# Performance work log

Measured on AMD Instinct MI355X. Metric: run time of the kernel, lower is better.

The kernel has to match this reference:

```python
import jax, jax.numpy as jnp
import numpy as np

N = 500_000
H = 256
G = 4096
NUM_TIMESTEPS = 2


def setup_inputs() -> dict:
    key = jax.random.key(0)
    ks = jax.random.split(key, 12)
    s = 0.05
    x = jax.random.normal(ks[0], (N, H), dtype=jnp.float32)
    batch = jnp.sort(jax.random.randint(ks[1], (N,), 0, G, dtype=jnp.int64))
    return {
        "x": x,
        "gate_w1": jax.random.normal(ks[2], (H, H), dtype=jnp.float32) * s,
        "gate_b1": jax.random.normal(ks[3], (H,), dtype=jnp.float32) * s,
        "gate_w2": jax.random.normal(ks[4], (1, H), dtype=jnp.float32) * s,
        "gate_b2": jax.random.normal(ks[5], (1,), dtype=jnp.float32) * s,
        "gru_w_ih": jax.random.normal(ks[6], (3 * H, H), dtype=jnp.float32) * s,
        "gru_w_hh": jax.random.normal(ks[7], (3 * H, H), dtype=jnp.float32) * s,
        "gru_b_ih": jax.random.normal(ks[8], (3 * H,), dtype=jnp.float32) * s,
        "gru_b_hh": jax.random.normal(ks[9], (3 * H,), dtype=jnp.float32) * s,
        "batch": batch,
        "num_graphs": G,
    }


def _gru_cell(inp, h, w_ih, w_hh, b_ih, b_hh):
    # torch.nn.GRUCell semantics; gate order [r, z, n]
    gi = inp @ w_ih.T + b_ih
    gh = h @ w_hh.T + b_hh
    i_r, i_z, i_n = jnp.split(gi, 3, axis=-1)
    h_r, h_z, h_n = jnp.split(gh, 3, axis=-1)
    r = jax.nn.sigmoid(i_r + h_r)
    z = jax.nn.sigmoid(i_z + h_z)
    n = jnp.tanh(i_n + r * h_n)
    return (1.0 - z) * n + z * h


def reference(x, gate_w1, gate_b1, gate_w2, gate_b2,
              gru_w_ih, gru_w_hh, gru_b_ih, gru_b_hh,
              batch, num_graphs):
    counts = jax.ops.segment_sum(jnp.ones((x.shape[0],), x.dtype), batch,
                                 num_segments=num_graphs)
    denom = jnp.maximum(counts, 1.0)[:, None]  # empty graphs -> 0 mean

    def mean_pool(v):
        return jax.ops.segment_sum(v, batch, num_segments=num_graphs) / denom

    graph_repr = mean_pool(x)  # (G, H)
    for _ in range(NUM_TIMESTEPS):
        # gather per-node graph context (batch is sorted == node_to_graph)
        gate_input = x + graph_repr[batch]  # (N, H)
        hgate = jax.nn.relu(gate_input @ gate_w1.T + gate_b1)
        gate = jax.nn.sigmoid(hgate @ gate_w2.T + gate_b2)  # (N, 1)
        weighted_x = x * gate
        new_graph_repr = mean_pool(weighted_x)
        graph_repr = _gru_cell(new_graph_repr, graph_repr,
                               gru_w_ih, gru_w_hh, gru_b_ih, gru_b_hh)
        graph_repr = jax.nn.relu(graph_repr)
    return graph_repr
```

## Files before the change

kernel.cpp:

```cpp
#include <hip/hip_runtime.h>
#include <hip/hip_bf16.h>
#include <stdint.h>

#define H 256
#define G 4096
#define TK 32
#define TP0 128

typedef __attribute__((ext_vector_type(8))) short bf16x8;
typedef __attribute__((ext_vector_type(4))) float f32x4;

__device__ inline short f2bf(float f){
  union { float f; uint32_t u; } v; v.f = f;
  uint32_t r = (v.u + 0x7FFFu + ((v.u >> 16) & 1u)) >> 16;
  return (short)(uint16_t)r;
}
__device__ inline float bf2f(short s){
  union { float f; uint32_t u; } v; v.u = ((uint32_t)(uint16_t)s) << 16;
  return v.f;
}
__device__ inline uint32_t pk2(float lo, float hi){
  return (uint32_t)(uint16_t)f2bf(lo) | ((uint32_t)(uint16_t)f2bf(hi) << 16);
}
__device__ inline uint32_t pkfp8(float4 v){
  int u = __builtin_amdgcn_cvt_pk_fp8_f32(v.x, v.y, 0, false);
  u = __builtin_amdgcn_cvt_pk_fp8_f32(v.z, v.w, u, true);
  return (uint32_t)u;
}
__device__ inline float sigmoidf_(float x){ return 1.f / (1.f + __expf(-x)); }

__device__ inline void ldsbar(){
  asm volatile("s_waitcnt lgkmcnt(0)" ::: "memory");
  __builtin_amdgcn_s_barrier();
}

__global__ void conv_w(const float* __restrict__ w1, const float* __restrict__ wih,
                       const float* __restrict__ whh,
                       short* __restrict__ o1, short* __restrict__ oih, short* __restrict__ ohh,
                       uint8_t* __restrict__ w1q,
                       float* __restrict__ counts, float* __restrict__ pool){
  int i = blockIdx.x * 256 + threadIdx.x;
  if (i < H*H) o1[i] = f2bf(w1[i]);
  if (i < 3*H*H){ oih[i] = f2bf(wih[i]); ohh[i] = f2bf(whh[i]); }
  if (i < H*H/4){
    float4 v = *(const float4*)(w1 + (size_t)i*4);
    *(uint32_t*)(w1q + (size_t)i*4) = pkfp8(v);
  }
  if (i < G) counts[i] = 0.f;
  for (int j = i; j < G*H; j += 768*256) pool[j] = 0.f;
}

__global__ __launch_bounds__(512) __attribute__((amdgpu_waves_per_eu(2, 8)))
void k0_pool(const float* __restrict__ x, const int* __restrict__ batch,
             float* __restrict__ pool, float* __restrict__ counts,
             short* __restrict__ xbf, uint8_t* __restrict__ xq,
             float* __restrict__ sgate, int nNodes){
  __shared__ int   ng[TP0];
  __shared__ float Pacc[8][H];
  __shared__ float Cacc[8];
  __shared__ int   spanSh;

  const int t = threadIdx.x;
  const int base = blockIdx.x * TP0;
  const int c4 = (t & 63) * 4;
  const int r0 = (t >> 6) * 16;

  float4 v[16];
  #pragma unroll
  for (int i = 0; i < 16; ++i){
    int node = base + r0 + i;
    if (node < nNodes) v[i] = *(const float4*)(x + (size_t)node*H + c4);
    else v[i] = make_float4(0.f,0.f,0.f,0.f);
  }

  { int gi = blockIdx.x * 512 + t; if (gi < nNodes) sgate[gi] = 0.f; }

  if (t < TP0) ng[t] = (base + t < nNodes) ? batch[base + t] : -1;
  for (int u = t; u < 8*H; u += 512) ((float*)Pacc)[u] = 0.f;
  if (t < 8) Cacc[t] = 0.f;
  __syncthreads();

  if (t == 0){
    int lg = ng[0];
    if (base + TP0 <= nNodes) lg = ng[TP0-1];
    else { for (int i = TP0-1; i > 0; --i){ if (ng[i] >= 0){ lg = ng[i]; break; } } }
    spanSh = (ng[0] >= 0) ? (lg - ng[0]) : -1;
  }

  if (xbf){
    #pragma unroll
    for (int i = 0; i < 16; ++i){
      int node = base + r0 + i;
      if (node < nNodes){
        ushort4 o;
        o.x = (uint16_t)f2bf(v[i].x); o.y = (uint16_t)f2bf(v[i].y);
        o.z = (uint16_t)f2bf(v[i].z); o.w = (uint16_t)f2bf(v[i].w);
        *(ushort4*)(xbf + (size_t)node*H + c4) = o;
        *(uint32_t*)(xq + (size_t)node*H + c4) = pkfp8(v[i]);
      }
    }
  }
  __syncthreads();

  const int g0 = ng[0];
  const bool useLds = (spanSh >= 0) && (spanSh < 8);

  float ax=0.f, ay=0.f, az=0.f, aw=0.f;
  int cur = ng[r0];
  if (cur >= 0){
    #pragma unroll
    for (int i = 0; i < 16; ++i){
      int g = ng[r0 + i];
      if (g < 0) break;
      if (g != cur){
        if (useLds){
          atomicAdd(&Pacc[cur-g0][c4], ax);   atomicAdd(&Pacc[cur-g0][c4+1], ay);
          atomicAdd(&Pacc[cur-g0][c4+2], az); atomicAdd(&Pacc[cur-g0][c4+3], aw);
        } else {
          atomicAdd(&pool[(size_t)cur*H + c4], ax);   atomicAdd(&pool[(size_t)cur*H + c4+1], ay);
          atomicAdd(&pool[(size_t)cur*H + c4+2], az); atomicAdd(&pool[(size_t)cur*H + c4+3], aw);
        }
        ax=ay=az=aw=0.f; cur = g;
      }
      ax += v[i].x; ay += v[i].y; az += v[i].z; aw += v[i].w;
    }
    if (useLds){
      atomicAdd(&Pacc[cur-g0][c4], ax);   atomicAdd(&Pacc[cur-g0][c4+1], ay);
      atomicAdd(&Pacc[cur-g0][c4+2], az); atomicAdd(&Pacc[cur-g0][c4+3], aw);
    } else {
      atomicAdd(&pool[(size_t)cur*H + c4], ax);   atomicAdd(&pool[(size_t)cur*H + c4+1], ay);
      atomicAdd(&pool[(size_t)cur*H + c4+2], az); atomicAdd(&pool[(size_t)cur*H + c4+3], aw);
    }
  }
  if (t < TP0 && ng[t] >= 0){
    if (useLds) atomicAdd(&Cacc[ng[t]-g0], 1.f);
    else        atomicAdd(&counts[ng[t]], 1.f);
  }
  __syncthreads();

  if (useLds){
    int nr = spanSh + 1;
    for (int u = t; u < nr*H; u += 512){
      int r = u >> 8, c = u & 255;
      float vv = Pacc[r][c];
      if (vv != 0.f) atomicAdd(&pool[(size_t)(g0+r)*H + c], vv);
    }
    if (t < nr && Cacc[t] != 0.f) atomicAdd(&counts[g0 + t], Cacc[t]);
  }
}

__global__ __launch_bounds__(256) void kT2(float* __restrict__ pool,
    const float* __restrict__ counts, float* __restrict__ repr,
    const short* __restrict__ w1bf, const float* __restrict__ b1,
    uint32_t* __restrict__ hgp){
  __shared__ short Ar[16][H + 8];
  const int t    = threadIdx.x;
  const int wid  = t >> 6;
  const int lane = t & 63;
  const int l15  = lane & 15;
  const int l4   = lane >> 4;
  const int g0   = blockIdx.x * 16;

  for (int u = t; u < 16*32; u += 256){
    int row = u >> 5, cg = u & 31;
    int c0 = cg * 8;
    int g = g0 + row;
    float cnt = fmaxf(counts[g], 1.f);
    float4* pp = (float4*)(pool + (size_t)g*H + c0);
    float4 p0 = pp[0], p1 = pp[1];
    p0.x/=cnt; p0.y/=cnt; p0.z/=cnt; p0.w/=cnt;
    p1.x/=cnt; p1.y/=cnt; p1.z/=cnt; p1.w/=cnt;
    float4* rp = (float4*)(repr + (size_t)g*H + c0);
    rp[0] = p0; rp[1] = p1;
    pp[0] = make_float4(0.f,0.f,0.f,0.f);
    pp[1] = make_float4(0.f,0.f,0.f,0.f);
    bf16x8 o;
    o[0]=f2bf(p0.x); o[1]=f2bf(p0.y); o[2]=f2bf(p0.z); o[3]=f2bf(p0.w);
    o[4]=f2bf(p1.x); o[5]=f2bf(p1.y); o[6]=f2bf(p1.z); o[7]=f2bf(p1.w);
    *(bf16x8*)(&Ar[row][c0]) = o;
  }
  __syncthreads();

  f32x4 acc[4];
  #pragma unroll
  for (int i = 0; i < 4; ++i) acc[i] = (f32x4){0.f,0.f,0.f,0.f};
  #pragma unroll
  for (int kc = 0; kc < 8; ++kc){
    bf16x8 a = *(bf16x8*)(&Ar[l15][kc*32 + l4*8]);
    #pragma unroll
    for (int nt = 0; nt < 4; ++nt){
      int col = wid*64 + nt*16 + l15;
      bf16x8 b = *(const bf16x8*)(w1bf + (size_t)col*H + kc*32 + l4*8);
      acc[nt] = __builtin_amdgcn_mfma_f32_16x16x32_bf16(a, b, acc[nt], 0, 0, 0);
    }
  }
  const float b1v0 = b1[wid*64 + l15];
  const float b1v1 = b1[wid*64 + 16 + l15];
  const float b1v2 = b1[wid*64 + 32 + l15];
  const float b1v3 = b1[wid*64 + 48 + l15];
  #pragma unroll
  for (int j = 0; j < 4; ++j){
    int row = l4*4 + j;
    hgp[(size_t)(g0+row)*128 + wid*32 + l15]      = pk2(acc[0][j]+b1v0, acc[1][j]+b1v1);
    hgp[(size_t)(g0+row)*128 + wid*32 + 16 + l15] = pk2(acc[2][j]+b1v2, acc[3][j]+b1v3);
  }
}

__global__ __launch_bounds__(256) __attribute__((amdgpu_waves_per_eu(3, 4)))
void k1a_fp8(
    const uint8_t* __restrict__ xq, const int* __restrict__ batch,
    const uint32_t* __restrict__ hgp, const uint8_t* __restrict__ w1q,
    const float* __restrict__ w2, float* __restrict__ sgate,
    int nNodes, int nTiles, int nBlk){

  __shared__ uint8_t Ain[2][TK][H + 16];
  __shared__ int     ngS[2][TK];

  const int t    = threadIdx.x;
  const int wid  = t >> 6;
  const int lane = t & 63;
  const int l15  = lane & 15;
  const int l4   = lane >> 4;
  const int colB = wid*64;

  const int tile0 = (int)(((long long)blockIdx.x * nTiles) / nBlk);
  const int tile1 = (int)(((long long)(blockIdx.x+1) * nTiles) / nBlk);
  if (tile0 >= tile1) return;

  long BfA0[8], BfA1[8], BfB0[8], BfB1[8];
  {
    const uint8_t* wp = w1q + (size_t)(colB + l15)*H + l4*8;
    #pragma unroll
    for (int kc = 0; kc < 8; ++kc){
      BfA0[kc] = *(const long*)(wp + kc*32);
      BfA1[kc] = *(const long*)(wp + 16*H + kc*32);
      BfB0[kc] = *(const long*)(wp + 32*H + kc*32);
      BfB1[kc] = *(const long*)(wp + 48*H + kc*32);
    }
  }
  const float w2A0 = w2[colB + l15];
  const float w2A1 = w2[colB + 16 + l15];
  const float w2B0 = w2[colB + 32 + l15];
  const float w2B1 = w2[colB + 48 + l15];

  const int srow  = t >> 4;
  const int scolB = (t & 15) * 16;
  uint4 xv0, xv1;
  int ngv = -1;

  auto issueT = [&](int tile){
    int base = tile * TK;
    int n0 = base + srow, n1 = n0 + 16;
    xv0 = (n0 < nNodes) ? *(const uint4*)(xq + (size_t)n0*H + scolB) : make_uint4(0,0,0,0);
    xv1 = (n1 < nNodes) ? *(const uint4*)(xq + (size_t)n1*H + scolB) : make_uint4(0,0,0,0);
    if (t < TK){
      int node = base + t;
      ngv = (node < nNodes) ? batch[node] : -1;
    }
  };
  auto stageT = [&](int buf){
    *(uint4*)(&Ain[buf][srow][scolB])      = xv0;
    *(uint4*)(&Ain[buf][srow + 16][scolB]) = xv1;
    if (t < TK) ngS[buf][t] = ngv;
  };

  issueT(tile0);
  stageT(0);
  if (tile0 + 1 < tile1) issueT(tile0 + 1);

  int cur = 0;
  for (int tile = tile0; tile < tile1; ++tile, cur ^= 1){
    ldsbar();

    uint32_t hvp[2][4];
    #pragma unroll
    for (int r = 0; r < 2; ++r)
      #pragma unroll
      for (int j = 0; j < 4; ++j){
        int g = ngS[cur][r*16 + l4*4 + j];
        hvp[r][j] = (g >= 0) ? hgp[(size_t)g*128 + wid*32 + l15] : 0u;
      }

    f32x4 acc0[2], acc1[2];
    #pragma unroll
    for (int r = 0; r < 2; ++r){ acc0[r] = (f32x4){0.f,0.f,0.f,0.f}; acc1[r] = (f32x4){0.f,0.f,0.f,0.f}; }
    #pragma unroll
    for (int kc = 0; kc < 8; ++kc){
      #pragma unroll
      for (int r = 0; r < 2; ++r){
        long a = *(const long*)(&Ain[cur][r*16 + l15][kc*32 + l4*8]);
        acc0[r] = __builtin_amdgcn_mfma_f32_16x16x32_fp8_fp8(a, BfA0[kc], acc0[r], 0, 0, 0);
        acc1[r] = __builtin_amdgcn_mfma_f32_16x16x32_fp8_fp8(a, BfA1[kc], acc1[r], 0, 0, 0);
      }
    }

    if (tile + 1 < tile1){
      stageT(cur ^ 1);
      if (tile + 2 < tile1) issueT(tile + 2);
    }

    float p[2][4];
    #pragma unroll
    for (int r = 0; r < 2; ++r)
      #pragma unroll
      for (int j = 0; j < 4; ++j){
        float h0 = fmaxf(acc0[r][j] + bf2f((short)(uint16_t)(hvp[r][j] & 0xFFFFu)), 0.f);
        float h1 = fmaxf(acc1[r][j] + bf2f((short)(uint16_t)(hvp[r][j] >> 16)), 0.f);
        p[r][j] = w2A0*h0 + w2A1*h1;
      }

    #pragma unroll
    for (int r = 0; r < 2; ++r)
      #pragma unroll
      for (int j = 0; j < 4; ++j){
        int g = ngS[cur][r*16 + l4*4 + j];
        hvp[r][j] = (g >= 0) ? hgp[(size_t)g*128 + wid*32 + 16 + l15] : 0u;
      }
    #pragma unroll
    for (int r = 0; r < 2; ++r){ acc0[r] = (f32x4){0.f,0.f,0.f,0.f}; acc1[r] = (f32x4){0.f,0.f,0.f,0.f}; }
    #pragma unroll
    for (int kc = 0; kc < 8; ++kc){
      #pragma unroll
      for (int r = 0; r < 2; ++r){
        long a = *(const long*)(&Ain[cur][r*16 + l15][kc*32 + l4*8]);
        acc0[r] = __builtin_amdgcn_mfma_f32_16x16x32_fp8_fp8(a, BfB0[kc], acc0[r], 0, 0, 0);
        acc1[r] = __builtin_amdgcn_mfma_f32_16x16x32_fp8_fp8(a, BfB1[kc], acc1[r], 0, 0, 0);
      }
    }
    #pragma unroll
    for (int r = 0; r < 2; ++r)
      #pragma unroll
      for (int j = 0; j < 4; ++j){
        float h0 = fmaxf(acc0[r][j] + bf2f((short)(uint16_t)(hvp[r][j] & 0xFFFFu)), 0.f);
        float h1 = fmaxf(acc1[r][j] + bf2f((short)(uint16_t)(hvp[r][j] >> 16)), 0.f);
        p[r][j] += w2B0*h0 + w2B1*h1;
      }

    #pragma unroll
    for (int off = 1; off < 16; off <<= 1){
      #pragma unroll
      for (int r = 0; r < 2; ++r)
        #pragma unroll
        for (int j = 0; j < 4; ++j) p[r][j] += __shfl_xor(p[r][j], off);
    }
    if (l15 == 0){
      int base = tile * TK;
      #pragma unroll
      for (int r = 0; r < 2; ++r)
        #pragma unroll
        for (int j = 0; j < 4; ++j){
          int idx = r*16 + l4*4 + j;
          if (ngS[cur][idx] >= 0)
            atomicAdd(&sgate[base + idx], p[r][j]);
        }
    }
  }
}

template<bool BF>
__global__ __launch_bounds__(512) __attribute__((amdgpu_waves_per_eu(2, 8)))
void k1b_pool(
    const float* __restrict__ xf32, const short* __restrict__ xbf,
    const int* __restrict__ batch, float* __restrict__ sgate,
    const float* __restrict__ b2p, float* __restrict__ pool, int nNodes){

  __shared__ int   ng[TP0];
  __shared__ float gs[TP0];
  __shared__ float Pacc[8][H];
  __shared__ int   spanSh;

  const int t = threadIdx.x;
  const int base = blockIdx.x * TP0;
  const int c4 = (t & 63) * 4;
  const int r0 = (t >> 6) * 16;

  ushort4 u[16];
  float4  vf[16];
  #pragma unroll
  for (int i = 0; i < 16; ++i){
    int node = base + r0 + i;
    if constexpr (BF){
      u[i] = (node < nNodes) ? *(const ushort4*)(xbf + (size_t)node*H + c4)
                             : make_ushort4(0,0,0,0);
    } else {
      vf[i] = (node < nNodes) ? *(const float4*)(xf32 + (size_t)node*H + c4)
                              : make_float4(0.f,0.f,0.f,0.f);
    }
  }

  const float b2v = b2p[0];
  if (t < TP0){
    int node = base + t;
    if (node < nNodes){
      ng[t] = batch[node];
      gs[t] = sigmoidf_(sgate[node] + b2v);
      sgate[node] = 0.f;
    } else { ng[t] = -1; gs[t] = 0.f; }
  }
  for (int w = t; w < 8*H; w += 512) ((float*)Pacc)[w] = 0.f;
  __syncthreads();

  if (t == 0){
    int lg = ng[0];
    if (base + TP0 <= nNodes) lg = ng[TP0-1];
    else { for (int i = TP0-1; i > 0; --i){ if (ng[i] >= 0){ lg = ng[i]; break; } } }
    spanSh = (ng[0] >= 0) ? (lg - ng[0]) : -1;
  }
  __syncthreads();

  const int g0 = ng[0];
  const bool useLds = (spanSh >= 0) && (spanSh < 8);

  float ax=0.f, ay=0.f, az=0.f, aw=0.f;
  int cur = ng[r0];
  if (cur >= 0){
    #pragma unroll
    for (int i = 0; i < 16; ++i){
      int g = ng[r0 + i];
      if (g < 0) break;
      if (g != cur){
        if (useLds){
          atomicAdd(&Pacc[cur-g0][c4], ax);   atomicAdd(&Pacc[cur-g0][c4+1], ay);
          atomicAdd(&Pacc[cur-g0][c4+2], az); atomicAdd(&Pacc[cur-g0][c4+3], aw);
        } else {
          atomicAdd(&pool[(size_t)cur*H + c4], ax);   atomicAdd(&pool[(size_t)cur*H + c4+1], ay);
          atomicAdd(&pool[(size_t)cur*H + c4+2], az); atomicAdd(&pool[(size_t)cur*H + c4+3], aw);
        }
        ax=ay=az=aw=0.f; cur = g;
      }
      float gv = gs[r0 + i];
      if constexpr (BF){
        ax += gv * bf2f((short)u[i].x); ay += gv * bf2f((short)u[i].y);
        az += gv * bf2f((short)u[i].z); aw += gv * bf2f((short)u[i].w);
      } else {
        ax += gv * bf2f(f2bf(vf[i].x)); ay += gv * bf2f(f2bf(vf[i].y));
        az += gv * bf2f(f2bf(vf[i].z)); aw += gv * bf2f(f2bf(vf[i].w));
      }
    }
    if (useLds){
      atomicAdd(&Pacc[cur-g0][c4], ax);   atomicAdd(&Pacc[cur-g0][c4+1], ay);
      atomicAdd(&Pacc[cur-g0][c4+2], az); atomicAdd(&Pacc[cur-g0][c4+3], aw);
    } else {
      atomicAdd(&pool[(size_t)cur*H + c4], ax);   atomicAdd(&pool[(size_t)cur*H + c4+1], ay);
      atomicAdd(&pool[(size_t)cur*H + c4+2], az); atomicAdd(&pool[(size_t)cur*H + c4+3], aw);
    }
  }
  __syncthreads();

  if (useLds){
    int nr = spanSh + 1;
    for (int w = t; w < nr*H; w += 512){
      int r = w >> 8, c = w & 255;
      float vv = Pacc[r][c];
      if (vv != 0.f) atomicAdd(&pool[(size_t)(g0+r)*H + c], vv);
    }
  }
}

__global__ __launch_bounds__(256) __attribute__((amdgpu_waves_per_eu(3, 4)))
void k1a_gate_f32(
    const float* __restrict__ xf32, const int* __restrict__ batch,
    const uint32_t* __restrict__ hgp, const short* __restrict__ w1bf,
    const float* __restrict__ w2, float* __restrict__ sgate,
    int nNodes, int nTiles, int nChains){

  __shared__ short Ain[2][TK][H + 8];
  __shared__ int   ngS[2][TK];

  const int t    = threadIdx.x;
  const int wid  = t >> 6;
  const int lane = t & 63;
  const int l15  = lane & 15;
  const int l4   = lane >> 4;

  const int ch    = blockIdx.x >= nChains;
  const int chain = ch ? blockIdx.x - nChains : blockIdx.x;
  const int colB  = ch*128 + wid*32;
  const int hgcol = ch*64 + wid*16 + l15;

  const int tile0 = (int)(((long long)chain * nTiles) / nChains);
  const int tile1 = (int)(((long long)(chain+1) * nTiles) / nChains);
  if (tile0 >= tile1) return;

  bf16x8 Bf0[8], Bf1[8];
  {
    const short* wp0 = w1bf + (size_t)(colB + l15)*H + l4*8;
    #pragma unroll
    for (int kc = 0; kc < 8; ++kc){
      Bf0[kc] = *(const bf16x8*)(wp0 + kc*32);
      Bf1[kc] = *(const bf16x8*)(wp0 + 16*H + kc*32);
    }
  }
  const float w2v0 = w2[colB + l15];
  const float w2v1 = w2[colB + 16 + l15];

  const int srow = t >> 5;
  const int scol = (t & 31) * 8;
  float4 xf[4][2];
  int ngv = -1;

  auto issueT = [&](int tile){
    int base = tile * TK;
    #pragma unroll
    for (int q = 0; q < 4; ++q){
      int node = base + srow + q*8;
      if (node < nNodes){
        const float4* xp = (const float4*)(xf32 + (size_t)node*H + scol);
        xf[q][0] = xp[0]; xf[q][1] = xp[1];
      } else { xf[q][0] = make_float4(0.f,0.f,0.f,0.f); xf[q][1] = make_float4(0.f,0.f,0.f,0.f); }
    }
    if (t < TK){
      int node = base + t;
      ngv = (node < nNodes) ? batch[node] : -1;
    }
  };
  auto stageT = [&](int buf){
    #pragma unroll
    for (int q = 0; q < 4; ++q){
      bf16x8 o;
      float4 a = xf[q][0], c = xf[q][1];
      o[0]=f2bf(a.x); o[1]=f2bf(a.y); o[2]=f2bf(a.z); o[3]=f2bf(a.w);
      o[4]=f2bf(c.x); o[5]=f2bf(c.y); o[6]=f2bf(c.z); o[7]=f2bf(c.w);
      *(bf16x8*)(&Ain[buf][srow + q*8][scol]) = o;
    }
    if (t < TK) ngS[buf][t] = ngv;
  };

  issueT(tile0);
  stageT(0);
  if (tile0 + 1 < tile1) issueT(tile0 + 1);

  int cur = 0;
  for (int tile = tile0; tile < tile1; ++tile, cur ^= 1){
    ldsbar();

    int gr[2][4];
    uint32_t hvp[2][4];
    #pragma unroll
    for (int r = 0; r < 2; ++r)
      #pragma unroll
      for (int j = 0; j < 4; ++j){
        int g = ngS[cur][r*16 + l4*4 + j];
        gr[r][j] = g;
        hvp[r][j] = (g >= 0) ? hgp[(size_t)g*128 + hgcol] : 0u;
      }

    f32x4 acc0[2], acc1[2];
    #pragma unroll
    for (int r = 0; r < 2; ++r){ acc0[r] = (f32x4){0.f,0.f,0.f,0.f}; acc1[r] = (f32x4){0.f,0.f,0.f,0.f}; }
    #pragma unroll
    for (int kc = 0; kc < 8; ++kc){
      #pragma unroll
      for (int r = 0; r < 2; ++r){
        bf16x8 a = *(bf16x8*)(&Ain[cur][r*16 + l15][kc*32 + l4*8]);
        acc0[r] = __builtin_amdgcn_mfma_f32_16x16x32_bf16(a, Bf0[kc], acc0[r], 0, 0, 0);
        acc1[r] = __builtin_amdgcn_mfma_f32_16x16x32_bf16(a, Bf1[kc], acc1[r], 0, 0, 0);
      }
    }

    if (tile + 1 < tile1){
      stageT(cur ^ 1);
      if (tile + 2 < tile1) issueT(tile + 2);
    }

    float p[2][4];
    #pragma unroll
    for (int r = 0; r < 2; ++r)
      #pragma unroll
      for (int j = 0; j < 4; ++j){
        float h0 = fmaxf(acc0[r][j] + bf2f((short)(uint16_t)(hvp[r][j] & 0xFFFFu)), 0.f);
        float h1 = fmaxf(acc1[r][j] + bf2f((short)(uint16_t)(hvp[r][j] >> 16)), 0.f);
        p[r][j] = w2v0*h0 + w2v1*h1;
      }
    #pragma unroll
    for (int off = 1; off < 16; off <<= 1){
      #pragma unroll
      for (int r = 0; r < 2; ++r)
        #pragma unroll
        for (int j = 0; j < 4; ++j) p[r][j] += __shfl_xor(p[r][j], off);
    }
    if (l15 == 0){
      int base = tile * TK;
      #pragma unroll
      for (int r = 0; r < 2; ++r)
        #pragma unroll
        for (int j = 0; j < 4; ++j){
          if (gr[r][j] >= 0)
            atomicAdd(&sgate[base + r*16 + l4*4 + j], p[r][j]);
        }
    }
  }
}

__global__ __launch_bounds__(256) void k2_gru(float* __restrict__ pool,
    const float* __restrict__ counts, const float* __restrict__ repr_in,
    const short* __restrict__ wihbf, const short* __restrict__ whhbf,
    const float* __restrict__ bih, const float* __restrict__ bhh,
    float* __restrict__ repr_out,
    const short* __restrict__ w1bf, const float* __restrict__ b1,
    uint32_t* __restrict__ hgp, int doHg){

  __shared__ short Anew[16][H + 8];
  __shared__ short Aold[16][H + 8];
  __shared__ float hold[16][H];
  __shared__ float srz[16][2*H];
  __shared__ float sni[16][H];
  __shared__ float snh[16][H];

  const int t    = threadIdx.x;
  const int wid  = t >> 6;
  const int lane = t & 63;
  const int l15  = lane & 15;
  const int l4   = lane >> 4;
  const int g0   = blockIdx.x * 16;

  for (int u = t; u < 16*H; u += 256){
    int row = u >> 8, c = u & 255;
    int g = g0 + row;
    float cnt = fmaxf(counts[g], 1.f);
    float rin = repr_in[(size_t)g*H + c];
    float nr  = pool[(size_t)g*H + c] / cnt;
    pool[(size_t)g*H + c] = 0.f;
    Anew[row][c] = f2bf(nr);
    Aold[row][c] = f2bf(rin);
    hold[row][c] = rin;
  }
  __syncthreads();

  f32x4 ai[12], ah[12];
  #pragma unroll
  for (int i = 0; i < 12; ++i){ ai[i] = (f32x4){0.f,0.f,0.f,0.f}; ah[i] = (f32x4){0.f,0.f,0.f,0.f}; }

  for (int kc = 0; kc < 8; ++kc){
    bf16x8 an = *(bf16x8*)(&Anew[l15][kc*32 + l4*8]);
    bf16x8 ao = *(bf16x8*)(&Aold[l15][kc*32 + l4*8]);
    #pragma unroll
    for (int nt = 0; nt < 12; ++nt){
      int n = wid*192 + nt*16 + l15;
      bf16x8 bi = *(const bf16x8*)(wihbf + (size_t)n*H + kc*32 + l4*8);
      bf16x8 bh = *(const bf16x8*)(whhbf + (size_t)n*H + kc*32 + l4*8);
      ai[nt] = __builtin_amdgcn_mfma_f32_16x16x32_bf16(an, bi, ai[nt], 0, 0, 0);
      ah[nt] = __builtin_amdgcn_mfma_f32_16x16x32_bf16(ao, bh, ah[nt], 0, 0, 0);
    }
  }

  #pragma unroll
  for (int nt = 0; nt < 12; ++nt){
    int n = wid*192 + nt*16 + l15;
    float bi = bih[n], bh = bhh[n];
    #pragma unroll
    for (int r = 0; r < 4; ++r){
      int row = l4*4 + r;
      float si = ai[nt][r] + bi;
      float sh = ah[nt][r] + bh;
      if (n < 2*H) srz[row][n] = si + sh;
      else { sni[row][n - 2*H] = si; snh[row][n - 2*H] = sh; }
    }
  }
  __syncthreads();

  for (int u = t; u < 16*H; u += 256){
    int row = u >> 8, c = u & 255;
    float rr = sigmoidf_(srz[row][c]);
    float zz = sigmoidf_(srz[row][H + c]);
    float nn = tanhf(sni[row][c] + rr * snh[row][c]);
    float hv = (1.f - zz) * nn + zz * hold[row][c];
    float out = fmaxf(hv, 0.f);
    repr_out[(size_t)(g0 + row)*H + c] = out;
    Anew[row][c] = f2bf(out);
  }

  if (doHg){
    __syncthreads();
    f32x4 acc[4];
    #pragma unroll
    for (int i = 0; i < 4; ++i) acc[i] = (f32x4){0.f,0.f,0.f,0.f};
    #pragma unroll
    for (int kc = 0; kc < 8; ++kc){
      bf16x8 a = *(bf16x8*)(&Anew[l15][kc*32 + l4*8]);
      #pragma unroll
      for (int nt = 0; nt < 4; ++nt){
        int col = wid*64 + nt*16 + l15;
        bf16x8 b = *(const bf16x8*)(w1bf + (size_t)col*H + kc*32 + l4*8);
        acc[nt] = __builtin_amdgcn_mfma_f32_16x16x32_bf16(a, b, acc[nt], 0, 0, 0);
      }
    }
    const float b1v0 = b1[wid*64 + l15];
    const float b1v1 = b1[wid*64 + 16 + l15];
    const float b1v2 = b1[wid*64 + 32 + l15];
    const float b1v3 = b1[wid*64 + 48 + l15];
    #pragma unroll
    for (int j = 0; j < 4; ++j){
      int row = l4*4 + j;
      hgp[(size_t)(g0+row)*128 + wid*32 + l15]      = pk2(acc[0][j]+b1v0, acc[1][j]+b1v1);
      hgp[(size_t)(g0+row)*128 + wid*32 + 16 + l15] = pk2(acc[2][j]+b1v2, acc[3][j]+b1v3);
    }
  }
}

extern "C" void kernel_launch(void* const* d_in, const int* in_sizes, int n_in,
                              void* d_out, int out_size, void* d_ws, size_t ws_size,
                              hipStream_t stream){
  const float* x    = (const float*)d_in[0];
  const float* w1   = (const float*)d_in[1];
  const float* b1   = (const float*)d_in[2];
  const float* w2   = (const float*)d_in[3];
  const float* b2   = (const float*)d_in[4];
  const float* wih  = (const float*)d_in[5];
  const float* whh  = (const float*)d_in[6];
  const float* bih  = (const float*)d_in[7];
  const float* bhh  = (const float*)d_in[8];
  const int*   batch= (const int*)d_in[9];
  const int N = in_sizes[9];

  char* ws = (char*)d_ws;
  short* w1bf   = (short*)(ws + 0);
  short* wihbf  = (short*)(ws + (1u<<17));
  short* whhbf  = (short*)(ws + (1u<<19));
  float* counts = (float*)(ws + 917504);
  uint8_t* w1q  = (uint8_t*)(ws + 933888);
  float* pool   = (float*)(ws + (1u<<20));
  float* repr   = (float*)(ws + (1u<<20) + (1u<<22));
  float* sgate  = (float*)(ws + (9u<<20));
  uint32_t* hgp = (uint32_t*)(ws + (12u<<20));
  float* outp   = (float*)d_out;

  const size_t XBF_OFF = (size_t)16u << 20;
  const size_t XQ_OFF  = XBF_OFF + ((size_t)272u << 20);
  const bool useXbf = ws_size >= XQ_OFF + (size_t)N * H;
  short*   xbf = useXbf ? (short*)(ws + XBF_OFF) : nullptr;
  uint8_t* xq  = useXbf ? (uint8_t*)(ws + XQ_OFF) : nullptr;

  const int nTiles  = (N + TK - 1) / TK;
  const int nBlk1a  = 1024;
  const int nChainsF= 512;
  const int nBlkP   = (N + TP0 - 1) / TP0;

  conv_w<<<768, 256, 0, stream>>>(w1, wih, whh, w1bf, wihbf, whhbf, w1q, counts, pool);
  k0_pool<<<nBlkP, 512, 0, stream>>>(x, batch, pool, counts, xbf, xq, sgate, N);
  kT2<<<G/16, 256, 0, stream>>>(pool, counts, repr, w1bf, b1, hgp);

  for (int ts = 0; ts < 2; ++ts){
    if (useXbf){
      k1a_fp8<<<nBlk1a, 256, 0, stream>>>(xq, batch, hgp, w1q, w2, sgate, N, nTiles, nBlk1a);
      k1b_pool<true><<<nBlkP, 512, 0, stream>>>(x, xbf, batch, sgate, b2, pool, N);
    } else {
      k1a_gate_f32<<<nChainsF*2, 256, 0, stream>>>(x, batch, hgp, w1bf, w2, sgate, N, nTiles, nChainsF);
      k1b_pool<false><<<nBlkP, 512, 0, stream>>>(x, xbf, batch, sgate, b2, pool, N);
    }
    k2_gru<<<G/16, 256, 0, stream>>>(pool, counts, repr, wihbf, whhbf, bih, bhh,
                                     (ts == 0) ? repr : outp,
                                     w1bf, b1, hgp, (ts == 0) ? 1 : 0);
  }
}
```

Measured before the change: 668.1 us.

## Fuse gate computation with weighted pooling using fp8 node features in-tile

The gate GEMM kernel now also applies the sigmoid gate and accumulates the weighted node features into the graph pool directly from its staged fp8 tile. It uses an LDS window of 16 graphs that is flushed to global memory with atomics. This removes the separate pooling pass, which reread x, and drops the bf16 copy of x. The trade-off is that pooling now uses fp8-quantized x instead of bf16 or fp32, which lowers accuracy, and it adds extra barriers and LDS traffic to the GEMM loop.

```diff
diff --git a/kernel.cpp b/kernel.cpp
--- a/kernel.cpp
+++ b/kernel.cpp
@@ -9,6 +9,7 @@
 
 typedef __attribute__((ext_vector_type(8))) short bf16x8;
 typedef __attribute__((ext_vector_type(4))) float f32x4;
+typedef __attribute__((ext_vector_type(2))) float f32x2;
 
 __device__ inline short f2bf(float f){
   union { float f; uint32_t u; } v; v.f = f;
@@ -53,8 +54,7 @@
 __global__ __launch_bounds__(512) __attribute__((amdgpu_waves_per_eu(2, 8)))
 void k0_pool(const float* __restrict__ x, const int* __restrict__ batch,
              float* __restrict__ pool, float* __restrict__ counts,
-             short* __restrict__ xbf, uint8_t* __restrict__ xq,
-             float* __restrict__ sgate, int nNodes){
+             uint8_t* __restrict__ xq, float* __restrict__ sgate, int nNodes){
   __shared__ int   ng[TP0];
   __shared__ float Pacc[8][H];
   __shared__ float Cacc[8];
@@ -87,17 +87,12 @@
     spanSh = (ng[0] >= 0) ? (lg - ng[0]) : -1;
   }
 
-  if (xbf){
+  if (xq){
     #pragma unroll
     for (int i = 0; i < 16; ++i){
       int node = base + r0 + i;
-      if (node < nNodes){
-        ushort4 o;
-        o.x = (uint16_t)f2bf(v[i].x); o.y = (uint16_t)f2bf(v[i].y);
-        o.z = (uint16_t)f2bf(v[i].z); o.w = (uint16_t)f2bf(v[i].w);
-        *(ushort4*)(xbf + (size_t)node*H + c4) = o;
+      if (node < nNodes)
         *(uint32_t*)(xq + (size_t)node*H + c4) = pkfp8(v[i]);
-      }
     }
   }
   __syncthreads();
@@ -207,14 +202,16 @@
 }
 
 __global__ __launch_bounds__(256) __attribute__((amdgpu_waves_per_eu(3, 4)))
-void k1a_fp8(
+void k1_fused(
     const uint8_t* __restrict__ xq, const int* __restrict__ batch,
     const uint32_t* __restrict__ hgp, const uint8_t* __restrict__ w1q,
-    const float* __restrict__ w2, float* __restrict__ sgate,
-    int nNodes, int nTiles, int nBlk){
+    const float* __restrict__ w2, const float* __restrict__ b2p,
+    float* __restrict__ pool, int nNodes, int nTiles, int nBlk){
 
   __shared__ uint8_t Ain[2][TK][H + 16];
   __shared__ int     ngS[2][TK];
+  __shared__ float   part[4][TK];
+  __shared__ float   Pacc[16][H];
 
   const int t    = threadIdx.x;
   const int wid  = t >> 6;
@@ -227,6 +224,8 @@
   const int tile1 = (int)(((long long)(blockIdx.x+1) * nTiles) / nBlk);
   if (tile0 >= tile1) return;
 
+  for (int u = t; u < 16*H; u += 256) ((float*)Pacc)[u] = 0.f;
+
   long BfA0[8], BfA1[8], BfB0[8], BfB1[8];
   {
     const uint8_t* wp = w1q + (size_t)(colB + l15)*H + l4*8;
@@ -242,6 +241,9 @@
   const float w2A1 = w2[colB + 16 + l15];
   const float w2B0 = w2[colB + 32 + l15];
   const float w2B1 = w2[colB + 48 + l15];
+  const float b2v  = b2p[0];
+
+  int gw0 = batch[tile0 * TK];
 
   const int srow  = t >> 4;
   const int scolB = (t & 15) * 16;
@@ -272,6 +274,25 @@
   for (int tile = tile0; tile < tile1; ++tile, cur ^= 1){
     ldsbar();
 
+    int gfirst = ngS[cur][0];
+    int glast;
+    if (tile*TK + TK <= nNodes) glast = ngS[cur][TK-1];
+    else {
+      glast = gfirst;
+      for (int i = TK-1; i > 0; --i){ if (ngS[cur][i] >= 0){ glast = ngS[cur][i]; break; } }
+    }
+    if (gfirst >= 0 && glast >= gw0 + 16){
+      for (int u = t; u < 16*H; u += 256){
+        float vv = ((float*)Pacc)[u];
+        if (vv != 0.f){
+          int r = u >> 8, c = u & 255;
+          atomicAdd(&pool[(size_t)(gw0 + r)*H + c], vv);
+          ((float*)Pacc)[u] = 0.f;
+        }
+      }
+      gw0 = gfirst;
+    }
+
     uint32_t hvp[2][4];
     #pragma unroll
     for (int r = 0; r < 2; ++r)
@@ -344,25 +365,206 @@
         for (int j = 0; j < 4; ++j) p[r][j] += __shfl_xor(p[r][j], off);
     }
     if (l15 == 0){
+      #pragma unroll
+      for (int r = 0; r < 2; ++r)
+        #pragma unroll
+        for (int j = 0; j < 4; ++j) part[wid][r*16 + l4*4 + j] = p[r][j];
+    }
+
+    ldsbar();
+
+    {
+      const int c4p = (t & 63) * 4;
+      const int rr0 = (t >> 6) * 8;
+
+      float ax = 0.f, ay = 0.f, az = 0.f, aw = 0.f;
+      int curg = ngS[cur][rr0];
+      if (curg >= 0){
+        #pragma unroll
+        for (int i = 0; i < 8; ++i){
+          int row = rr0 + i;
+          int g = ngS[cur][row];
+          if (g < 0) break;
+          if (g != curg){
+            int idx = curg - gw0;
+            if (idx >= 0 && idx < 16){
+              atomicAdd(&Pacc[idx][c4p], ax);   atomicAdd(&Pacc[idx][c4p+1], ay);
+              atomicAdd(&Pacc[idx][c4p+2], az); atomicAdd(&Pacc[idx][c4p+3], aw);
+            } else {
+              atomicAdd(&pool[(size_t)curg*H + c4p], ax);   atomicAdd(&pool[(size_t)curg*H + c4p+1], ay);
+              atomicAdd(&pool[(size_t)curg*H + c4p+2], az); atomicAdd(&pool[(size_t)curg*H + c4p+3], aw);
+            }
+            ax = ay = az = aw = 0.f; curg = g;
+          }
+          float gate = sigmoidf_(part[0][row] + part[1][row] + part[2][row] + part[3][row] + b2v);
+          uint32_t w = *(const uint32_t*)(&Ain[cur][row][c4p]);
+          f32x2 lo = __builtin_amdgcn_cvt_pk_f32_fp8((int)w, false);
+          f32x2 hi = __builtin_amdgcn_cvt_pk_f32_fp8((int)w, true);
+          ax += gate * lo[0]; ay += gate * lo[1];
+          az += gate * hi[0]; aw += gate * hi[1];
+        }
+        int idx = curg - gw0;
+        if (idx >= 0 && idx < 16){
+          atomicAdd(&Pacc[idx][c4p], ax);   atomicAdd(&Pacc[idx][c4p+1], ay);
+          atomicAdd(&Pacc[idx][c4p+2], az); atomicAdd(&Pacc[idx][c4p+3], aw);
+        } else {
+          atomicAdd(&pool[(size_t)curg*H + c4p], ax);   atomicAdd(&pool[(size_t)curg*H + c4p+1], ay);
+          atomicAdd(&pool[(size_t)curg*H + c4p+2], az); atomicAdd(&pool[(size_t)curg*H + c4p+3], aw);
+        }
+      }
+    }
+  }
+
+  ldsbar();
+  for (int u = t; u < 16*H; u += 256){
+    float vv = ((float*)Pacc)[u];
+    if (vv != 0.f){
+      int r = u >> 8, c = u & 255;
+      atomicAdd(&pool[(size_t)(gw0 + r)*H + c], vv);
+    }
+  }
+}
+
+__global__ __launch_bounds__(256) __attribute__((amdgpu_waves_per_eu(3, 4)))
+void k1a_gate_f32(
+    const float* __restrict__ xf32, const int* __restrict__ batch,
+    const uint32_t* __restrict__ hgp, const short* __restrict__ w1bf,
+    const float* __restrict__ w2, float* __restrict__ sgate,
+    int nNodes, int nTiles, int nChains){
+
+  __shared__ short Ain[2][TK][H + 8];
+  __shared__ int   ngS[2][TK];
+
+  const int t    = threadIdx.x;
+  const int wid  = t >> 6;
+  const int lane = t & 63;
+  const int l15  = lane & 15;
+  const int l4   = lane >> 4;
+
+  const int ch    = blockIdx.x >= nChains;
+  const int chain = ch ? blockIdx.x - nChains : blockIdx.x;
+  const int colB  = ch*128 + wid*32;
+  const int hgcol = ch*64 + wid*16 + l15;
+
+  const int tile0 = (int)(((long long)chain * nTiles) / nChains);
+  const int tile1 = (int)(((long long)(chain+1) * nTiles) / nChains);
+  if (tile0 >= tile1) return;
+
+  bf16x8 Bf0[8], Bf1[8];
+  {
+    const short* wp0 = w1bf + (size_t)(colB + l15)*H + l4*8;
+    #pragma unroll
+    for (int kc = 0; kc < 8; ++kc){
+      Bf0[kc] = *(const bf16x8*)(wp0 + kc*32);
+      Bf1[kc] = *(const bf16x8*)(wp0 + 16*H + kc*32);
+    }
+  }
+  const float w2v0 = w2[colB + l15];
+  const float w2v1 = w2[colB + 16 + l15];
+
+  const int srow = t >> 5;
+  const int scol = (t & 31) * 8;
+  float4 xf[4][2];
+  int ngv = -1;
+
+  auto issueT = [&](int tile){
+    int base = tile * TK;
+    #pragma unroll
+    for (int q = 0; q < 4; ++q){
+      int node = base + srow + q*8;
+      if (node < nNodes){
+        const float4* xp = (const float4*)(xf32 + (size_t)node*H + scol);
+        xf[q][0] = xp[0]; xf[q][1] = xp[1];
+      } else { xf[q][0] = make_float4(0.f,0.f,0.f,0.f); xf[q][1] = make_float4(0.f,0.f,0.f,0.f); }
+    }
+    if (t < TK){
+      int node = base + t;
+      ngv = (node < nNodes) ? batch[node] : -1;
+    }
+  };
+  auto stageT = [&](int buf){
+    #pragma unroll
+    for (int q = 0; q < 4; ++q){
+      bf16x8 o;
+      float4 a = xf[q][0], c = xf[q][1];
+      o[0]=f2bf(a.x); o[1]=f2bf(a.y); o[2]=f2bf(a.z); o[3]=f2bf(a.w);
+      o[4]=f2bf(c.x); o[5]=f2bf(c.y); o[6]=f2bf(c.z); o[7]=f2bf(c.w);
+      *(bf16x8*)(&Ain[buf][srow + q*8][scol]) = o;
+    }
+    if (t < TK) ngS[buf][t] = ngv;
+  };
+
+  issueT(tile0);
+  stageT(0);
+  if (tile0 + 1 < tile1) issueT(tile0 + 1);
+
+  int cur = 0;
+  for (int tile = tile0; tile < tile1; ++tile, cur ^= 1){
+    ldsbar();
+
+    int gr[2][4];
+    uint32_t hvp[2][4];
+    #pragma unroll
+    for (int r = 0; r < 2; ++r)
+      #pragma unroll
+      for (int j = 0; j < 4; ++j){
+        int g = ngS[cur][r*16 + l4*4 + j];
+        gr[r][j] = g;
+        hvp[r][j] = (g >= 0) ? hgp[(size_t)g*128 + hgcol] : 0u;
+      }
+
+    f32x4 acc0[2], acc1[2];
+    #pragma unroll
+    for (int r = 0; r < 2; ++r){ acc0[r] = (f32x4){0.f,0.f,0.f,0.f}; acc1[r] = (f32x4){0.f,0.f,0.f,0.f}; }
+    #pragma unroll
+    for (int kc = 0; kc < 8; ++kc){
+      #pragma unroll
+      for (int r = 0; r < 2; ++r){
+        bf16x8 a = *(bf16x8*)(&Ain[cur][r*16 + l15][kc*32 + l4*8]);
+        acc0[r] = __builtin_amdgcn_mfma_f32_16x16x32_bf16(a, Bf0[kc], acc0[r], 0, 0, 0);
+        acc1[r] = __builtin_amdgcn_mfma_f32_16x16x32_bf16(a, Bf1[kc], acc1[r], 0, 0, 0);
+      }
+    }
+
+    if (tile + 1 < tile1){
+      stageT(cur ^ 1);
+      if (tile + 2 < tile1) issueT(tile + 2);
+    }
+
+    float p[2][4];
+    #pragma unroll
+    for (int r = 0; r < 2; ++r)
+      #pragma unroll
+      for (int j = 0; j < 4; ++j){
+        float h0 = fmaxf(acc0[r][j] + bf2f((short)(uint16_t)(hvp[r][j] & 0xFFFFu)), 0.f);
+        float h1 = fmaxf(acc1[r][j] + bf2f((short)(uint16_t)(hvp[r][j] >> 16)), 0.f);
+        p[r][j] = w2v0*h0 + w2v1*h1;
+      }
+    #pragma unroll
+    for (int off = 1; off < 16; off <<= 1){
+      #pragma unroll
+      for (int r = 0; r < 2; ++r)
+        #pragma unroll
+        for (int j = 0; j < 4; ++j) p[r][j] += __shfl_xor(p[r][j], off);
+    }
+    if (l15 == 0){
       int base = tile * TK;
       #pragma unroll
       for (int r = 0; r < 2; ++r)
         #pragma unroll
         for (int j = 0; j < 4; ++j){
-          int idx = r*16 + l4*4 + j;
-          if (ngS[cur][idx] >= 0)
-            atomicAdd(&sgate[base + idx], p[r][j]);
+          if (gr[r][j] >= 0)
+            atomicAdd(&sgate[base + r*16 + l4*4 + j], p[r][j]);
         }
     }
   }
 }
 
-template<bool BF>
 __global__ __launch_bounds__(512) __attribute__((amdgpu_waves_per_eu(2, 8)))
 void k1b_pool(
-    const float* __restrict__ xf32, const short* __restrict__ xbf,
-    const int* __restrict__ batch, float* __restrict__ sgate,
-    const float* __restrict__ b2p, float* __restrict__ pool, int nNodes){
+    const float* __restrict__ xf32, const int* __restrict__ batch,
+    float* __restrict__ sgate, const float* __restrict__ b2p,
+    float* __restrict__ pool, int nNodes){
 
   __shared__ int   ng[TP0];
   __shared__ float gs[TP0];
@@ -374,18 +576,12 @@
   const int c4 = (t & 63) * 4;
   const int r0 = (t >> 6) * 16;
 
-  ushort4 u[16];
-  float4  vf[16];
+  float4 vf[16];
   #pragma unroll
   for (int i = 0; i < 16; ++i){
     int node = base + r0 + i;
-    if constexpr (BF){
-      u[i] = (node < nNodes) ? *(const ushort4*)(xbf + (size_t)node*H + c4)
-                             : make_ushort4(0,0,0,0);
-    } else {
-      vf[i] = (node < nNodes) ? *(const float4*)(xf32 + (size_t)node*H + c4)
-                              : make_float4(0.f,0.f,0.f,0.f);
-    }
+    vf[i] = (node < nNodes) ? *(const float4*)(xf32 + (size_t)node*H + c4)
+                            : make_float4(0.f,0.f,0.f,0.f);
   }
 
   const float b2v = b2p[0];
@@ -429,13 +625,8 @@
         ax=ay=az=aw=0.f; cur = g;
       }
       float gv = gs[r0 + i];
-      if constexpr (BF){
-        ax += gv * bf2f((short)u[i].x); ay += gv * bf2f((short)u[i].y);
-        az += gv * bf2f((short)u[i].z); aw += gv * bf2f((short)u[i].w);
-      } else {
-        ax += gv * bf2f(f2bf(vf[i].x)); ay += gv * bf2f(f2bf(vf[i].y));
-        az += gv * bf2f(f2bf(vf[i].z)); aw += gv * bf2f(f2bf(vf[i].w));
-      }
+      ax += gv * bf2f(f2bf(vf[i].x)); ay += gv * bf2f(f2bf(vf[i].y));
+      az += gv * bf2f(f2bf(vf[i].z)); aw += gv * bf2f(f2bf(vf[i].w));
     }
     if (useLds){
       atomicAdd(&Pacc[cur-g0][c4], ax);   atomicAdd(&Pacc[cur-g0][c4+1], ay);
@@ -453,141 +644,6 @@
       int r = w >> 8, c = w & 255;
       float vv = Pacc[r][c];
       if (vv != 0.f) atomicAdd(&pool[(size_t)(g0+r)*H + c], vv);
-    }
-  }
-}
-
-__global__ __launch_bounds__(256) __attribute__((amdgpu_waves_per_eu(3, 4)))
-void k1a_gate_f32(
-    const float* __restrict__ xf32, const int* __restrict__ batch,
-    const uint32_t* __restrict__ hgp, const short* __restrict__ w1bf,
-    const float* __restrict__ w2, float* __restrict__ sgate,
-    int nNodes, int nTiles, int nChains){
-
-  __shared__ short Ain[2][TK][H + 8];
-  __shared__ int   ngS[2][TK];
-
-  const int t    = threadIdx.x;
-  const int wid  = t >> 6;
-  const int lane = t & 63;
-  const int l15  = lane & 15;
-  const int l4   = lane >> 4;
-
-  const int ch    = blockIdx.x >= nChains;
-  const int chain = ch ? blockIdx.x - nChains : blockIdx.x;
-  const int colB  = ch*128 + wid*32;
-  const int hgcol = ch*64 + wid*16 + l15;
-
-  const int tile0 = (int)(((long long)chain * nTiles) / nChains);
-  const int tile1 = (int)(((long long)(chain+1) * nTiles) / nChains);
-  if (tile0 >= tile1) return;
-
-  bf16x8 Bf0[8], Bf1[8];
-  {
-    const short* wp0 = w1bf + (size_t)(colB + l15)*H + l4*8;
-    #pragma unroll
-    for (int kc = 0; kc < 8; ++kc){
-      Bf0[kc] = *(const bf16x8*)(wp0 + kc*32);
-      Bf1[kc] = *(const bf16x8*)(wp0 + 16*H + kc*32);
-    }
-  }
-  const float w2v0 = w2[colB + l15];
-  const float w2v1 = w2[colB + 16 + l15];
-
-  const int srow = t >> 5;
-  const int scol = (t & 31) * 8;
-  float4 xf[4][2];
-  int ngv = -1;
-
-  auto issueT = [&](int tile){
-    int base = tile * TK;
-    #pragma unroll
-    for (int q = 0; q < 4; ++q){
-      int node = base + srow + q*8;
-      if (node < nNodes){
-        const float4* xp = (const float4*)(xf32 + (size_t)node*H + scol);
-        xf[q][0] = xp[0]; xf[q][1] = xp[1];
-      } else { xf[q][0] = make_float4(0.f,0.f,0.f,0.f); xf[q][1] = make_float4(0.f,0.f,0.f,0.f); }
-    }
-    if (t < TK){
-      int node = base + t;
-      ngv = (node < nNodes) ? batch[node] : -1;
-    }
-  };
-  auto stageT = [&](int buf){
-    #pragma unroll
-    for (int q = 0; q < 4; ++q){
-      bf16x8 o;
-      float4 a = xf[q][0], c = xf[q][1];
-      o[0]=f2bf(a.x); o[1]=f2bf(a.y); o[2]=f2bf(a.z); o[3]=f2bf(a.w);
-      o[4]=f2bf(c.x); o[5]=f2bf(c.y); o[6]=f2bf(c.z); o[7]=f2bf(c.w);
-      *(bf16x8*)(&Ain[buf][srow + q*8][scol]) = o;
-    }
-    if (t < TK) ngS[buf][t] = ngv;
-  };
-
-  issueT(tile0);
-  stageT(0);
-  if (tile0 + 1 < tile1) issueT(tile0 + 1);
-
-  int cur = 0;
-  for (int tile = tile0; tile < tile1; ++tile, cur ^= 1){
-    ldsbar();
-
-    int gr[2][4];
-    uint32_t hvp[2][4];
-    #pragma unroll
-    for (int r = 0; r < 2; ++r)
-      #pragma unroll
-      for (int j = 0; j < 4; ++j){
-        int g = ngS[cur][r*16 + l4*4 + j];
-        gr[r][j] = g;
-        hvp[r][j] = (g >= 0) ? hgp[(size_t)g*128 + hgcol] : 0u;
-      }
-
-    f32x4 acc0[2], acc1[2];
-    #pragma unroll
-    for (int r = 0; r < 2; ++r){ acc0[r] = (f32x4){0.f,0.f,0.f,0.f}; acc1[r] = (f32x4){0.f,0.f,0.f,0.f}; }
-    #pragma unroll
-    for (int kc = 0; kc < 8; ++kc){
-      #pragma unroll
-      for (int r = 0; r < 2; ++r){
-        bf16x8 a = *(bf16x8*)(&Ain[cur][r*16 + l15][kc*32 + l4*8]);
-        acc0[r] = __builtin_amdgcn_mfma_f32_16x16x32_bf16(a, Bf0[kc], acc0[r], 0, 0, 0);
-        acc1[r] = __builtin_amdgcn_mfma_f32_16x16x32_bf16(a, Bf1[kc], acc1[r], 0, 0, 0);
-      }
-    }
-
-    if (tile + 1 < tile1){
-      stageT(cur ^ 1);
-      if (tile + 2 < tile1) issueT(tile + 2);
-    }
-
-    float p[2][4];
-    #pragma unroll
-    for (int r = 0; r < 2; ++r)
-      #pragma unroll
-      for (int j = 0; j < 4; ++j){
-        float h0 = fmaxf(acc0[r][j] + bf2f((short)(uint16_t)(hvp[r][j] & 0xFFFFu)), 0.f);
-        float h1 = fmaxf(acc1[r][j] + bf2f((short)(uint16_t)(hvp[r][j] >> 16)), 0.f);
-        p[r][j] = w2v0*h0 + w2v1*h1;
-      }
-    #pragma unroll
-    for (int off = 1; off < 16; off <<= 1){
-      #pragma unroll
-      for (int r = 0; r < 2; ++r)
-        #pragma unroll
-        for (int j = 0; j < 4; ++j) p[r][j] += __shfl_xor(p[r][j], off);
-    }
-    if (l15 == 0){
-      int base = tile * TK;
-      #pragma unroll
-      for (int r = 0; r < 2; ++r)
-        #pragma unroll
-        for (int j = 0; j < 4; ++j){
-          if (gr[r][j] >= 0)
-            atomicAdd(&sgate[base + r*16 + l4*4 + j], p[r][j]);
-        }
     }
   }
 }
@@ -725,28 +781,25 @@
   uint32_t* hgp = (uint32_t*)(ws + (12u<<20));
   float* outp   = (float*)d_out;
 
-  const size_t XBF_OFF = (size_t)16u << 20;
-  const size_t XQ_OFF  = XBF_OFF + ((size_t)272u << 20);
-  const bool useXbf = ws_size >= XQ_OFF + (size_t)N * H;
-  short*   xbf = useXbf ? (short*)(ws + XBF_OFF) : nullptr;
-  uint8_t* xq  = useXbf ? (uint8_t*)(ws + XQ_OFF) : nullptr;
+  const size_t XQ_OFF = (size_t)16u << 20;
+  const bool useXq = ws_size >= XQ_OFF + (size_t)N * H;
+  uint8_t* xq = useXq ? (uint8_t*)(ws + XQ_OFF) : nullptr;
 
   const int nTiles  = (N + TK - 1) / TK;
-  const int nBlk1a  = 1024;
+  const int nBlk1   = 1024;
   const int nChainsF= 512;
   const int nBlkP   = (N + TP0 - 1) / TP0;
 
   conv_w<<<768, 256, 0, stream>>>(w1, wih, whh, w1bf, wihbf, whhbf, w1q, counts, pool);
-  k0_pool<<<nBlkP, 512, 0, stream>>>(x, batch, pool, counts, xbf, xq, sgate, N);
+  k0_pool<<<nBlkP, 512, 0, stream>>>(x, batch, pool, counts, xq, sgate, N);
   kT2<<<G/16, 256, 0, stream>>>(pool, counts, repr, w1bf, b1, hgp);
 
   for (int ts = 0; ts < 2; ++ts){
-    if (useXbf){
-      k1a_fp8<<<nBlk1a, 256, 0, stream>>>(xq, batch, hgp, w1q, w2, sgate, N, nTiles, nBlk1a);
-      k1b_pool<true><<<nBlkP, 512, 0, stream>>>(x, xbf, batch, sgate, b2, pool, N);
+    if (useXq){
+      k1_fused<<<nBlk1, 256, 0, stream>>>(xq, batch, hgp, w1q, w2, b2, pool, N, nTiles, nBlk1);
     } else {
       k1a_gate_f32<<<nChainsF*2, 256, 0, stream>>>(x, batch, hgp, w1bf, w2, sgate, N, nTiles, nChainsF);
-      k1b_pool<false><<<nBlkP, 512, 0, stream>>>(x, xbf, batch, sgate, b2, pool, N);
+      k1b_pool<<<nBlkP, 512, 0, stream>>>(x, batch, sgate, b2, pool, N);
     }
     k2_gru<<<G/16, 256, 0, stream>>>(pool, counts, repr, wihbf, whhbf, bih, bhh,
                                      (ts == 0) ? repr : outp,
```

Result: slower. 758.9 us (+13.6%).
